# Performance work log

Measured on AMD Instinct MI355X. Metric: run time of the kernel, lower is better.

## Reference

```python
import jax, jax.numpy as jnp
import numpy as np

HEADS = 8
DIM_HEAD = 64


def setup_inputs() -> dict:
    key = jax.random.key(0)
    ks = jax.random.split(key, 6)
    B, Nq, Nk, Dq = 4, 2048, 2048, 1024
    inner = HEADS * DIM_HEAD  # 512
    return {
        "x": jax.random.normal(ks[0], (B, Nq, Dq), jnp.float32),
        "context": jax.random.normal(ks[1], (B, Nk, Dq), jnp.float32),
        "Wq": jax.random.normal(ks[2], (Dq, inner), jnp.float32) * 0.02,
        "Wkv": jax.random.normal(ks[3], (Dq, 2 * inner), jnp.float32) * 0.02,
        "Wout": jax.random.normal(ks[4], (inner, Dq), jnp.float32) * 0.02,
        "bout": jax.random.normal(ks[5], (Dq,), jnp.float32) * 0.02,
        "topk": 64,
    }


def reference(x, context, Wq, Wkv, Wout, bout, topk):
    B, Nq, _ = x.shape
    Nk = context.shape[1]
    H, D = HEADS, DIM_HEAD
    scale = D ** -0.5

    # projections: b n (h d) -> b h n d
    q = (x @ Wq).reshape(B, Nq, H, D).transpose(0, 2, 1, 3)
    kv = context @ Wkv
    k, v = jnp.split(kv, 2, axis=-1)
    k = k.reshape(B, Nk, H, D).transpose(0, 2, 1, 3)
    v = v.reshape(B, Nk, H, D).transpose(0, 2, 1, 3)

    sim = jnp.einsum('bhid,bhjd->bhij', q, k) * scale  # [B,H,Nq,Nk]

    # top-k sparsification: keep only topk keys per query, mask rest to -max
    k_eff = min(int(topk), Nk)
    _, idx = jax.lax.top_k(sim, k_eff)  # [B,H,Nq,k_eff]
    keep = jnp.zeros(sim.shape, dtype=bool)
    bi = jnp.arange(B)[:, None, None, None]
    hi = jnp.arange(H)[None, :, None, None]
    qi = jnp.arange(Nq)[None, None, :, None]
    keep = keep.at[bi, hi, qi, idx].set(True)
    max_neg = -jnp.finfo(sim.dtype).max
    sim = jnp.where(keep, sim, max_neg)

    attn = jax.nn.softmax(sim, axis=-1)
    out = jnp.einsum('bhij,bhjd->bhid', attn, v)
    out = out.transpose(0, 2, 1, 3).reshape(B, Nq, H * D)
    return out @ Wout + bout
```

## Files before the change

### kernel.cpp

```cpp
#include <hip/hip_runtime.h>
#include <math.h>

#define BATCH 4
#define NQ 2048
#define NK 2048
#define DQ 1024
#define NHEADS 8
#define DHEAD 64
#define INNER (NHEADS*DHEAD)
#define NROWS (BATCH*NHEADS*NQ)
#define CAND_MAX 128

using frag_ab = __attribute__((ext_vector_type(8))) short;
using frag_cd = __attribute__((ext_vector_type(4))) float;
using u16x8   = __attribute__((ext_vector_type(8))) unsigned short;

static __device__ __forceinline__ unsigned short f32_to_bf16_rne(float f) {
  unsigned u = __float_as_uint(f);
  u += 0x7FFFu + ((u >> 16) & 1u);
  return (unsigned short)(u >> 16);
}

static __device__ __forceinline__ void split_trunc(float f, unsigned short& h, unsigned short& l) {
  unsigned u = __float_as_uint(f);
  h = (unsigned short)(u >> 16);
  float hf = __uint_as_float(u & 0xFFFF0000u);
  unsigned r = __float_as_uint(f - hf);
  l = (unsigned short)(r >> 16);
}

static __device__ __forceinline__ void split3(float f, unsigned short& h,
                                              unsigned short& m, unsigned short& l) {
  unsigned u = __float_as_uint(f);
  h = (unsigned short)(u >> 16);
  float hf = __uint_as_float(u & 0xFFFF0000u);
  float r1 = f - hf;
  unsigned u1 = __float_as_uint(r1);
  m = (unsigned short)(u1 >> 16);
  float mf = __uint_as_float(u1 & 0xFFFF0000u);
  float r2 = r1 - mf;
  l = (unsigned short)(__float_as_uint(r2) >> 16);
}

__global__ __launch_bounds__(256) void split_wT3(
    const float* __restrict__ W, int ldw, int coloff, int K, int N,
    unsigned short* __restrict__ TH, unsigned short* __restrict__ TM,
    unsigned short* __restrict__ TL)
{
  __shared__ float tile[32*33];
  const int k0 = blockIdx.x * 32, n0 = blockIdx.y * 32;
  const int t = threadIdx.x;
  {
    int lk = t >> 3, ln4 = (t & 7) * 4;
    const float4 v = *(const float4*)(W + (size_t)(k0 + lk)*ldw + coloff + n0 + ln4);
    tile[lk*33 + ln4+0] = v.x;
    tile[lk*33 + ln4+1] = v.y;
    tile[lk*33 + ln4+2] = v.z;
    tile[lk*33 + ln4+3] = v.w;
  }
  __syncthreads();
  int n = t >> 3, k4 = (t & 7) * 4;
  #pragma unroll
  for (int j = 0; j < 4; ++j) {
    unsigned short h, m, l;
    split3(tile[(k4+j)*33 + n], h, m, l);
    size_t o = (size_t)(n0 + n)*K + k0 + k4 + j;
    TH[o] = h; TM[o] = m; TL[o] = l;
  }
}

__global__ __launch_bounds__(256) void split_wT(
    const float* __restrict__ W, int ldw, int coloff, int K, int N,
    unsigned short* __restrict__ TH, unsigned short* __restrict__ TL)
{
  __shared__ float tile[32*33];
  const int k0 = blockIdx.x * 32, n0 = blockIdx.y * 32;
  const int t = threadIdx.x;
  {
    int lk = t >> 3, ln4 = (t & 7) * 4;
    const float4 v = *(const float4*)(W + (size_t)(k0 + lk)*ldw + coloff + n0 + ln4);
    tile[lk*33 + ln4+0] = v.x;
    tile[lk*33 + ln4+1] = v.y;
    tile[lk*33 + ln4+2] = v.z;
    tile[lk*33 + ln4+3] = v.w;
  }
  __syncthreads();
  int n = t >> 3, k4 = (t & 7) * 4;
  #pragma unroll
  for (int j = 0; j < 4; ++j) {
    unsigned short h, l;
    split_trunc(tile[(k4+j)*33 + n], h, l);
    TH[(size_t)(n0 + n)*K + k0 + k4 + j] = h;
    TL[(size_t)(n0 + n)*K + k0 + k4 + j] = l;
  }
}

__global__ __launch_bounds__(512) void gemm_mfma6_proj(
    const float* __restrict__ A0,
    const unsigned short* __restrict__ BtH0, const unsigned short* __restrict__ BtM0,
    const unsigned short* __restrict__ BtL0,
    float* __restrict__ C0_, unsigned short* __restrict__ Hi0, unsigned short* __restrict__ Lo0,
    const float* __restrict__ A1,
    const unsigned short* __restrict__ BtH1, const unsigned short* __restrict__ BtM1,
    const unsigned short* __restrict__ BtL1,
    float* __restrict__ C1_, unsigned short* __restrict__ Hi1, unsigned short* __restrict__ Lo1)
{
  extern __shared__ unsigned short smp[];
  unsigned short* ah = smp;
  unsigned short* am = ah + 128*40;
  unsigned short* al = am + 128*40;
  unsigned short* bh = al + 128*40;
  unsigned short* bm = bh + 128*40;
  unsigned short* bl = bm + 128*40;

  const int t = threadIdx.x;
  const int w = t >> 6, l = t & 63;
  const int lr = l & 15, quad = l >> 4;
  const int bid = (int)blockIdx.x;
  const int half = bid >> 8;
  const int b2 = bid & 255;
  const int lid = (b2 & 7) * 32 + (b2 >> 3);
  const int n0 = (lid & 3) * 128, m0 = (lid >> 2) * 128;

  const float* A = half ? A1 : A0;
  const unsigned short* BtH = half ? BtH1 : BtH0;
  const unsigned short* BtM = half ? BtM1 : BtM0;
  const unsigned short* BtL = half ? BtL1 : BtL0;
  float* C32 = half ? C1_ : C0_;
  unsigned short* Hi = half ? Hi1 : Hi0;
  unsigned short* Lo = half ? Lo1 : Lo0;

  frag_cd acc[8];
  #pragma unroll
  for (int nt = 0; nt < 8; ++nt)
    acc[nt] = (frag_cd){0.f, 0.f, 0.f, 0.f};

  for (int kt = 0; kt < DQ; kt += 32) {
    {
      int row = t >> 2, k8 = (t & 3) * 8;
      const float* src = A + (size_t)(m0 + row) * DQ + kt + k8;
      float4 v0 = *(const float4*)(src);
      float4 v1 = *(const float4*)(src + 4);
      float vv[8] = {v0.x, v0.y, v0.z, v0.w, v1.x, v1.y, v1.z, v1.w};
      unsigned short h8[8], m8[8], l8[8];
      #pragma unroll
      for (int j = 0; j < 8; ++j) split3(vv[j], h8[j], m8[j], l8[j]);
      *(u16x8*)(ah + row*40 + k8) = *(u16x8*)h8;
      *(u16x8*)(am + row*40 + k8) = *(u16x8*)m8;
      *(u16x8*)(al + row*40 + k8) = *(u16x8*)l8;
    }
    {
      int n = t >> 2, k8 = (t & 3) * 8;
      size_t o = (size_t)(n0 + n)*DQ + kt + k8;
      *(u16x8*)(bh + n*40 + k8) = *(const u16x8*)(BtH + o);
      *(u16x8*)(bm + n*40 + k8) = *(const u16x8*)(BtM + o);
      *(u16x8*)(bl + n*40 + k8) = *(const u16x8*)(BtL + o);
    }
    __syncthreads();
    {
      int row = w*16 + lr;
      frag_ab aH = *(const frag_ab*)(ah + row*40 + quad*8);
      frag_ab aM = *(const frag_ab*)(am + row*40 + quad*8);
      frag_ab aL = *(const frag_ab*)(al + row*40 + quad*8);
      #pragma unroll
      for (int nt = 0; nt < 8; ++nt) {
        int bn = nt*16 + lr;
        frag_ab bH_ = *(const frag_ab*)(bh + bn*40 + quad*8);
        frag_ab bM_ = *(const frag_ab*)(bm + bn*40 + quad*8);
        frag_ab bL_ = *(const frag_ab*)(bl + bn*40 + quad*8);
        frag_cd c = acc[nt];
        c = __builtin_amdgcn_mfma_f32_16x16x32_bf16(aL, bH_, c, 0, 0, 0);
        c = __builtin_amdgcn_mfma_f32_16x16x32_bf16(aH, bL_, c, 0, 0, 0);
        c = __builtin_amdgcn_mfma_f32_16x16x32_bf16(aM, bM_, c, 0, 0, 0);
        c = __builtin_amdgcn_mfma_f32_16x16x32_bf16(aM, bH_, c, 0, 0, 0);
        c = __builtin_amdgcn_mfma_f32_16x16x32_bf16(aH, bM_, c, 0, 0, 0);
        c = __builtin_amdgcn_mfma_f32_16x16x32_bf16(aH, bH_, c, 0, 0, 0);
        acc[nt] = c;
      }
    }
    __syncthreads();
  }

  #pragma unroll
  for (int nt = 0; nt < 8; ++nt) {
    int cc = n0 + nt*16 + lr;
    int h = cc >> 6, d = cc & 63;
    #pragma unroll
    for (int i = 0; i < 4; ++i) {
      int r = m0 + w*16 + quad*4 + i;
      int b = r >> 11, n = r & (NQ - 1);
      size_t idx = (((size_t)(b*NHEADS + h))*NQ + n)*64 + d;
      float vf = acc[nt][i];
      C32[idx] = vf;
      unsigned short hb = f32_to_bf16_rne(vf);
      float hf = __uint_as_float((unsigned)hb << 16);
      unsigned short lb = f32_to_bf16_rne(vf - hf);
      Hi[idx] = hb;
      Lo[idx] = lb;
    }
  }
}

template<int MODE>
__global__ __launch_bounds__(512) void gemm_mfma3(
    const float* __restrict__ A, int lda,
    const unsigned short* __restrict__ BtH, const unsigned short* __restrict__ BtL,
    int K, int N, const float* __restrict__ bias, float* __restrict__ C0)
{
  __shared__ unsigned short ah[128*40];
  __shared__ unsigned short al[128*40];
  __shared__ unsigned short bh2[128*40];
  __shared__ unsigned short bl2[128*40];
  const int t = threadIdx.x;
  const int w = t >> 6, l = t & 63;
  const int lr = l & 15, quad = l >> 4;
  const int nx = N >> 7;
  const int bid = (int)blockIdx.x;
  const int nwg = (int)gridDim.x;
  const int lid = (bid & 7) * (nwg >> 3) + (bid >> 3);
  const int n0 = (lid % nx) * 128, m0 = (lid / nx) * 128;

  frag_cd acc[8];
  #pragma unroll
  for (int nt = 0; nt < 8; ++nt)
    acc[nt] = (frag_cd){0.f, 0.f, 0.f, 0.f};

  for (int kt = 0; kt < K; kt += 32) {
    {
      int row = t >> 2, k8 = (t & 3) * 8;
      const float* src = A + (size_t)(m0 + row) * lda + kt + k8;
      float4 v0 = *(const float4*)(src);
      float4 v1 = *(const float4*)(src + 4);
      float vv[8] = {v0.x, v0.y, v0.z, v0.w, v1.x, v1.y, v1.z, v1.w};
      unsigned short h8[8], l8[8];
      #pragma unroll
      for (int j = 0; j < 8; ++j) split_trunc(vv[j], h8[j], l8[j]);
      *(u16x8*)(ah + row*40 + k8) = *(u16x8*)h8;
      *(u16x8*)(al + row*40 + k8) = *(u16x8*)l8;
    }
    {
      int n = t >> 2, k8 = (t & 3) * 8;
      size_t o = (size_t)(n0 + n)*K + kt + k8;
      *(u16x8*)(bh2 + n*40 + k8) = *(const u16x8*)(BtH + o);
      *(u16x8*)(bl2 + n*40 + k8) = *(const u16x8*)(BtL + o);
    }
    __syncthreads();
    {
      int row = w*16 + lr;
      frag_ab aH = *(const frag_ab*)(ah + row*40 + quad*8);
      frag_ab aL = *(const frag_ab*)(al + row*40 + quad*8);
      #pragma unroll
      for (int nt = 0; nt < 8; ++nt) {
        int bn = nt*16 + lr;
        frag_ab bH_ = *(const frag_ab*)(bh2 + bn*40 + quad*8);
        frag_ab bL_ = *(const frag_ab*)(bl2 + bn*40 + quad*8);
        acc[nt] = __builtin_amdgcn_mfma_f32_16x16x32_bf16(aH, bH_, acc[nt], 0, 0, 0);
        acc[nt] = __builtin_amdgcn_mfma_f32_16x16x32_bf16(aH, bL_, acc[nt], 0, 0, 0);
        acc[nt] = __builtin_amdgcn_mfma_f32_16x16x32_bf16(aL, bH_, acc[nt], 0, 0, 0);
      }
    }
    __syncthreads();
  }

  #pragma unroll
  for (int nt = 0; nt < 8; ++nt) {
    int cc = n0 + nt*16 + lr;
    #pragma unroll
    for (int i = 0; i < 4; ++i) {
      int r = m0 + w*16 + quad*4 + i;
      float v = acc[nt][i];
      if (MODE == 0) {
        C0[(size_t)r * N + cc] = v + bias[cc];
      } else {
        int b = r >> 11, n = r & (NQ - 1);
        int h = cc >> 6, d = cc & 63;
        C0[(((size_t)(b*NHEADS + h))*NK + n)*64 + d] = v;
      }
    }
  }
}

__global__ __launch_bounds__(512) void score_mfma(
    const unsigned short* __restrict__ Qhi, const unsigned short* __restrict__ Qlo,
    const unsigned short* __restrict__ Khi, const unsigned short* __restrict__ Klo,
    unsigned short* __restrict__ S16, int bh0)
{
  extern __shared__ unsigned short sm[];
  unsigned short* qh = sm;
  unsigned short* ql = qh + 128*72;
  unsigned short* kh = ql + 128*72;
  unsigned short* kl = kh + 128*72;

  const int t  = threadIdx.x;
  const int qt = blockIdx.x, kt = blockIdx.y;
  const int bh = bh0 + blockIdx.z;
  const size_t qbase = ((size_t)bh*NQ + qt*128) * 64;
  const size_t kbase = ((size_t)bh*NK + kt*128) * 64;

  #pragma unroll
  for (int i = 0; i < 2; ++i) {
    int c   = t + i*512;
    int row = c >> 3, off = (c & 7) * 8;
    *(u16x8*)(qh + row*72 + off) = *(const u16x8*)(Qhi + qbase + row*64 + off);
    *(u16x8*)(ql + row*72 + off) = *(const u16x8*)(Qlo + qbase + row*64 + off);
    *(u16x8*)(kh + row*72 + off) = *(const u16x8*)(Khi + kbase + row*64 + off);
    *(u16x8*)(kl + row*72 + off) = *(const u16x8*)(Klo + kbase + row*64 + off);
  }
  __syncthreads();

  const int w = t >> 6, l = t & 63;
  const int quad = l >> 4, lr = l & 15;

  frag_ab aH[2], aL[2];
  {
    int row = w*16 + lr;
    #pragma unroll
    for (int s = 0; s < 2; ++s) {
      aH[s] = *(const frag_ab*)(qh + row*72 + s*32 + quad*8);
      aL[s] = *(const frag_ab*)(ql + row*72 + s*32 + quad*8);
    }
  }

  for (int ks = 0; ks < 8; ++ks) {
    frag_ab bH[2], bL[2];
    int krow = ks*16 + lr;
    #pragma unroll
    for (int s = 0; s < 2; ++s) {
      bH[s] = *(const frag_ab*)(kh + krow*72 + s*32 + quad*8);
      bL[s] = *(const frag_ab*)(kl + krow*72 + s*32 + quad*8);
    }
    frag_cd c = {0.f, 0.f, 0.f, 0.f};
    #pragma unroll
    for (int s = 0; s < 2; ++s) {
      c = __builtin_amdgcn_mfma_f32_16x16x32_bf16(aH[s], bH[s], c, 0, 0, 0);
      c = __builtin_amdgcn_mfma_f32_16x16x32_bf16(aH[s], bL[s], c, 0, 0, 0);
      c = __builtin_amdgcn_mfma_f32_16x16x32_bf16(aL[s], bH[s], c, 0, 0, 0);
    }
    int qrow = qt*128 + w*16 + quad*4;
    int kcol = kt*128 + ks*16 + lr;
    size_t base = ((size_t)blockIdx.z * NQ + qrow) * NK + kcol;
    #pragma unroll
    for (int i = 0; i < 4; ++i) {
      _Float16 h = (_Float16)(c[i] * 0.125f);
      S16[base + (size_t)i*NK] = __builtin_bit_cast(unsigned short, h);
    }
  }
}

__global__ __launch_bounds__(256) void select_rows(
    const unsigned short* __restrict__ S16, unsigned short* __restrict__ cand,
    int* __restrict__ cnt, const int* __restrict__ topkp, int row0)
{
  const int t = threadIdx.x;
  const int w = t >> 6, l = t & 63;
  const int rl = blockIdx.x * 4 + w;
  const size_t row = (size_t)row0 + rl;
  const unsigned short* Sr = S16 + (size_t)rl * NK;
  const unsigned long long lmask = (1ull << l) - 1ull;

  int kEff = *topkp;
  if (kEff > CAND_MAX) kEff = CAND_MAX;
  if (kEff < 1) kEff = 1;

  unsigned uv[32];
  #pragma unroll
  for (int c = 0; c < 32; ++c) {
    unsigned bb = Sr[c*64 + l];
    uv[c] = (bb & 0x8000u) ? (~bb & 0xFFFFu) : (bb | 0x8000u);
  }
  unsigned lo_ = 0u, hi_ = 0xFFFFu;
  while (lo_ < hi_) {
    unsigned mid = (lo_ + hi_ + 1u) >> 1;
    int c_ = 0;
    #pragma unroll
    for (int c = 0; c < 32; ++c) c_ += (uv[c] >= mid) ? 1 : 0;
    #pragma unroll
    for (int off = 32; off > 0; off >>= 1) c_ += __shfl_xor(c_, off);
    if (c_ >= kEff) lo_ = mid; else hi_ = mid - 1;
  }
  unsigned short sb = (lo_ & 0x8000u) ? (unsigned short)(lo_ & 0x7FFFu)
                                      : (unsigned short)(~lo_ & 0xFFFFu);
  float skth = (float)__builtin_bit_cast(_Float16, sb);
  float smarg = skth - 3e-3f;
  _Float16 hm = (_Float16)smarg;
  unsigned short mb = __builtin_bit_cast(unsigned short, hm);
  unsigned um = (mb & 0x8000u) ? (~(unsigned)mb & 0xFFFFu) : ((unsigned)mb | 0x8000u);

  int base = 0;
  for (int c = 0; c < 32; ++c) {
    bool pred = (uv[c] >= um);
    unsigned long long msk = __ballot(pred);
    if (pred) {
      int pos = base + __popcll(msk & lmask);
      if (pos < CAND_MAX) cand[row*CAND_MAX + pos] = (unsigned short)(c*64 + l);
    }
    base += __popcll(msk);
  }
  if (l == 0) cnt[row] = (base < CAND_MAX) ? base : CAND_MAX;
}

__global__ __launch_bounds__(256) void attn_phase_b(
    const float* __restrict__ Q32, const float* __restrict__ K32,
    const float* __restrict__ V32, const unsigned short* __restrict__ cand,
    const int* __restrict__ cnt, float* __restrict__ inner,
    const int* __restrict__ topkp)
{
  __shared__ uint2 pvbuf[4][128];

  const int t = threadIdx.x;
  const int w = t >> 6, l = t & 63;
  const int nwg = (int)gridDim.x;
  const int bid = (int)blockIdx.x;
  const int swz = (bid & 7) * (nwg >> 3) + (bid >> 3);
  const size_t row = (size_t)swz * 4 + w;
  const int bh = (int)(row >> 11);
  const int q  = (int)(row & (NQ - 1));
  const unsigned long long lmask = (1ull << l) - 1ull;

  int kEff = *topkp;
  if (kEff > CAND_MAX) kEff = CAND_MAX;
  if (kEff < 1) kEff = 1;
  int m = cnt[row];
  if (kEff > m) kEff = m;

  const float* Kb = K32 + (size_t)bh * NK * 64;
  const float* Vb = V32 + (size_t)bh * NK * 64;

  const int g = l >> 3, r = l & 7;
  double2 q2[4];
  #pragma unroll
  for (int i = 0; i < 4; ++i) {
    float2 qf = *(const float2*)(Q32 + row*64 + i*16 + r*2);
    q2[i].x = (double)qf.x;
    q2[i].y = (double)qf.y;
  }

  int ck[2];
  ck[0] = cand[row*CAND_MAX + l];
  ck[1] = cand[row*CAND_MAX + 64 + l];
  double cs[2] = {-INFINITY, -INFINITY};
  unsigned long long cu[2] = {0ull, 0ull};

  #define RESCORE_PASS(P, C)                                                  \
  {                                                                           \
    const int j = (P)*8 + g;                                                  \
    const bool valid = (j < m);                                               \
    int key = __shfl(ck[C], j & 63);                                          \
    const float* kp = Kb + (size_t)(valid ? key : 0) * 64;                    \
    double s0 = 0.0, s1 = 0.0;                                                \
    _Pragma("unroll")                                                         \
    for (int i = 0; i < 4; ++i) {                                             \
      float2 kv = *(const float2*)(kp + i*16 + r*2);                          \
      s0 = fma((double)kv.x, q2[i].x, s0);                                    \
      s1 = fma((double)kv.y, q2[i].y, s1);                                    \
    }                                                                         \
    double s = s0 + s1;                                                       \
    s += __shfl_xor(s, 1);                                                    \
    s += __shfl_xor(s, 2);                                                    \
    s += __shfl_xor(s, 4);                                                    \
    s *= 0.125;                                                               \
    double sc = __shfl(s, (l & 7) * 8);                                       \
    const int pp = (P) & 7;                                                   \
    if ((l >> 3) == pp && ((C)*64 + pp*8 + (l & 7)) < m) {                    \
      unsigned long long b = (unsigned long long)__double_as_longlong(sc);    \
      cs[C] = sc;                                                             \
      cu[C] = (b >> 63) ? ~b : (b | 0x8000000000000000ull);                   \
    }                                                                         \
  }

  if (m <= 64) {
    #pragma unroll
    for (int p = 0; p < 8; ++p) RESCORE_PASS(p, 0)
  } else {
    #pragma unroll
    for (int p = 0; p < 8; ++p) RESCORE_PASS(p, 0)
    const int np2 = 8 + ((m - 64 + 7) >> 3);
    for (int p = 8; p < np2; ++p) RESCORE_PASS(p, 1)
  }
  #undef RESCORE_PASS

  const unsigned hu0 = (unsigned)(cu[0] >> 32), lu0 = (unsigned)cu[0];
  const unsigned hu1 = (unsigned)(cu[1] >> 32), lu1 = (unsigned)cu[1];

  unsigned T32 = 0u;
  for (int bit = 31; bit >= 0; --bit) {
    unsigned cT = T32 | (1u << bit);
    int tot = __popcll(__ballot(hu0 >= cT)) + __popcll(__ballot(hu1 >= cT));
    if (tot >= kEff) T32 = cT;
  }
  unsigned Tlo;
  {
    int cgt32 = __popcll(__ballot(hu0 > T32)) + __popcll(__ballot(hu1 > T32));
    bool e0 = (hu0 == T32), e1 = (hu1 == T32);
    unsigned long long bm0 = __ballot(e0), bm1 = __ballot(e1);
    int ceq = __popcll(bm0) + __popcll(bm1);
    int nEq32 = kEff - cgt32;
    if (ceq == 1) {
      Tlo = bm0 ? __shfl(lu0, (int)__builtin_ctzll(bm0))
                : __shfl(lu1, (int)__builtin_ctzll(bm1));
    } else {
      unsigned TL = 0u;
      for (int bit = 31; bit >= 0; --bit) {
        unsigned cT = TL | (1u << bit);
        int tot = __popcll(__ballot(e0 && lu0 >= cT))
                + __popcll(__ballot(e1 && lu1 >= cT));
        if (tot >= nEq32) TL = cT;
      }
      Tlo = TL;
    }
  }
  const unsigned long long T = ((unsigned long long)T32 << 32) | Tlo;

  double s_kth;
  { unsigned long long bb = (T >> 63) ? (T & 0x7FFFFFFFFFFFFFFFull) : ~T;
    s_kth = __longlong_as_double((long long)bb); }

  double nx = -INFINITY;
  #pragma unroll
  for (int c = 0; c < 2; ++c) { double v = (cu[c] < T) ? cs[c] : -INFINITY; nx = fmax(nx, v); }
  #pragma unroll
  for (int off = 32; off > 0; off >>= 1) nx = fmax(nx, __shfl_xor(nx, off));

  double smax = fmax(cs[0], cs[1]);
  #pragma unroll
  for (int off = 32; off > 0; off >>= 1) smax = fmax(smax, __shfl_xor(smax, off));

  const double DELTA = 5e-6;
  float wgt[2];
  if (!(s_kth - nx < 2.0*DELTA)) {
    int cgt = __popcll(__ballot(cu[0] > T)) + __popcll(__ballot(cu[1] > T));
    int nEq = kEff - cgt;
    int eqBase = 0;
    #pragma unroll
    for (int c = 0; c < 2; ++c) {
      bool eq = (cu[c] == T);
      unsigned long long eqm = __ballot(eq);
      int er = __popcll(eqm & lmask);
      bool sel = (cu[c] > T) || (eq && (eqBase + er) < nEq);
      eqBase += __popcll(eqm);
      wgt[c] = sel ? expf((float)(cs[c] - smax)) : 0.f;
    }
  } else {
    double cmid = 0.5 * (s_kth + nx);
    #pragma unroll
    for (int c = 0; c < 2; ++c) {
      double mu = 0.5 + (cs[c] - cmid) / (2.0*DELTA);
      mu = fmin(1.0, fmax(0.0, mu));
      wgt[c] = (float)mu * expf((float)(cs[c] - smax));
    }
  }

  pvbuf[w][l]      = make_uint2((unsigned)ck[0] & (NK - 1), __float_as_uint(wgt[0]));
  pvbuf[w][64 + l] = make_uint2((unsigned)ck[1] & (NK - 1), __float_as_uint(wgt[1]));
  float wsum = wgt[0] + wgt[1];
  #pragma unroll
  for (int off = 32; off > 0; off >>= 1) wsum += __shfl_xor(wsum, off);
  asm volatile("s_waitcnt lgkmcnt(0)" ::: "memory");

  const int sub = l >> 4;
  const int dl  = l & 15;
  const float* Vb4 = Vb + dl * 4;
  float ax = 0.f, ay = 0.f, az = 0.f, aw = 0.f;
  const int mm4 = (m + 3) & ~3;
  #pragma unroll 4
  for (int j0 = 0; j0 < mm4; j0 += 4) {
    uint2 p = pvbuf[w][j0 + sub];
    float wj = __uint_as_float(p.y);
    const float4 v = *(const float4*)(Vb4 + ((size_t)p.x << 6));
    ax = fmaf(wj, v.x, ax);
    ay = fmaf(wj, v.y, ay);
    az = fmaf(wj, v.z, az);
    aw = fmaf(wj, v.w, aw);
  }
  #pragma unroll
  for (int off = 32; off >= 16; off >>= 1) {
    ax += __shfl_xor(ax, off);
    ay += __shfl_xor(ay, off);
    az += __shfl_xor(az, off);
    aw += __shfl_xor(aw, off);
  }
  if (sub == 0) {
    int b = bh >> 3, h = bh & 7;
    float inv = 1.0f / wsum;
    float4 o;
    o.x = ax * inv; o.y = ay * inv; o.z = az * inv; o.w = aw * inv;
    *(float4*)(inner + ((size_t)b*NQ + q)*INNER + h*DHEAD + dl*4) = o;
  }
}

extern "C" void kernel_launch(void* const* d_in, const int* in_sizes, int n_in,
                              void* d_out, int out_size, void* d_ws, size_t ws_size,
                              hipStream_t stream)
{
  const float* x    = (const float*)d_in[0];
  const float* ctx  = (const float*)d_in[1];
  const float* Wq   = (const float*)d_in[2];
  const float* Wkv  = (const float*)d_in[3];
  const float* Wout = (const float*)d_in[4];
  const float* bout = (const float*)d_in[5];
  const int*   topk = (const int*)d_in[6];
  float* out = (float*)d_out;

  const size_t SZ = (size_t)BATCH * NHEADS * NQ * DHEAD;

  size_t off = 0;
  char* base = (char*)d_ws;
  auto take = [&](size_t bytes) { char* r = base + off; off += (bytes + 255) & ~(size_t)255; return r; };
  float* Q32 = (float*)take(SZ * sizeof(float));
  float* K32 = (float*)take(SZ * sizeof(float));
  unsigned short* cand = (unsigned short*)take((size_t)NROWS * CAND_MAX * 2);
  int* cnt = (int*)take((size_t)NROWS * sizeof(int));
  unsigned short* Qhi = (unsigned short*)take(SZ * 2);
  unsigned short* Qlo = (unsigned short*)take(SZ * 2);
  unsigned short* Khi = (unsigned short*)take(SZ * 2);
  unsigned short* Klo = (unsigned short*)take(SZ * 2);
  char* slab = base + off;

  const size_t WSZ = (size_t)INNER * DQ * 2;
  unsigned short* WqTH = (unsigned short*)(slab + 0*WSZ);
  unsigned short* WqTM = (unsigned short*)(slab + 1*WSZ);
  unsigned short* WqTL = (unsigned short*)(slab + 2*WSZ);
  unsigned short* WkTH = (unsigned short*)(slab + 3*WSZ);
  unsigned short* WkTM = (unsigned short*)(slab + 4*WSZ);
  unsigned short* WkTL = (unsigned short*)(slab + 5*WSZ);
  unsigned short* S16 = (unsigned short*)slab;
  unsigned short* WvTH = (unsigned short*)(slab + 0*WSZ);
  unsigned short* WvTL = (unsigned short*)(slab + 1*WSZ);
  unsigned short* WoTH = (unsigned short*)(slab + 2*WSZ);
  unsigned short* WoTL = (unsigned short*)(slab + 3*WSZ);
  float* V32   = (float*)Qhi;
  float* inner = (float*)Khi;

  const size_t per_bh = (size_t)NQ * NK * sizeof(unsigned short);
  size_t avail = (ws_size > off) ? (ws_size - off) : 0;
  int bhchunk = (int)(avail / per_bh);
  if (bhchunk < 1)  bhchunk = 1;
  if (bhchunk > 32) bhchunk = 32;

  const int M = BATCH * NQ;
  const int SCORE_LDS = 4 * 128 * 72 * (int)sizeof(unsigned short);
  const int PROJ_LDS  = 6 * 128 * 40 * (int)sizeof(unsigned short);
  hipFuncSetAttribute(reinterpret_cast<const void*>(score_mfma),
                      hipFuncAttributeMaxDynamicSharedMemorySize, SCORE_LDS);
  hipFuncSetAttribute(reinterpret_cast<const void*>(gemm_mfma6_proj),
                      hipFuncAttributeMaxDynamicSharedMemorySize, PROJ_LDS);

  split_wT3<<<dim3(DQ/32, INNER/32), 256, 0, stream>>>(Wq,  INNER,   0, DQ, INNER, WqTH, WqTM, WqTL);
  split_wT3<<<dim3(DQ/32, INNER/32), 256, 0, stream>>>(Wkv, 2*INNER, 0, DQ, INNER, WkTH, WkTM, WkTL);

  gemm_mfma6_proj<<<dim3(512), 512, PROJ_LDS, stream>>>(
      x,   WqTH, WqTM, WqTL, Q32, Qhi, Qlo,
      ctx, WkTH, WkTM, WkTL, K32, Khi, Klo);

  for (int c0 = 0; c0 < BATCH*NHEADS; c0 += bhchunk) {
    int cc = BATCH*NHEADS - c0; if (cc > bhchunk) cc = bhchunk;
    score_mfma<<<dim3(NQ/128, NK/128, cc), 512, SCORE_LDS, stream>>>(
        Qhi, Qlo, Khi, Klo, S16, c0);
    select_rows<<<dim3(cc*NQ/4), 256, 0, stream>>>(S16, cand, cnt, topk, c0*NQ);
  }

  split_wT<<<dim3(DQ/32, INNER/32), 256, 0, stream>>>(Wkv, 2*INNER, INNER, DQ, INNER, WvTH, WvTL);
  split_wT<<<dim3(INNER/32, DQ/32), 256, 0, stream>>>(Wout, DQ, 0, INNER, DQ, WoTH, WoTL);

  gemm_mfma3<2><<<dim3((INNER/128)*(M/128)), 512, 0, stream>>>(ctx, DQ, WvTH, WvTL, DQ, INNER, nullptr, V32);
  attn_phase_b<<<dim3(NROWS/4), 256, 0, stream>>>(Q32, K32, V32, cand, cnt, inner, topk);
  gemm_mfma3<0><<<dim3((DQ/128)*(M/128)), 512, 0, stream>>>(inner, INNER, WoTH, WoTL, INNER, DQ, bout, out);
}
```

Measured before the change: 708.8 us.

## Fuse score computation with top-k selection, keeping score rows in LDS

Merges the score GEMM and row-wise threshold selection into one kernel. Each block computes a 16-query by 2048-key score strip and holds it in shared memory, then runs the binary-search selection directly from LDS. This removes the large fp16 score matrix round trip through global memory and the chunked launch loop. In exchange, K fragments are read straight from global memory with no LDS reuse across query tiles, and each block uses about 70 KB of LDS, which limits occupancy.

```diff
diff --git a/kernel.cpp b/kernel.cpp
--- a/kernel.cpp
+++ b/kernel.cpp
@@ -280,54 +280,56 @@
   }
 }
 
-__global__ __launch_bounds__(512) void score_mfma(
+#define SC_STRIDE 2056
+__global__ __launch_bounds__(512) void score_select_fused(
     const unsigned short* __restrict__ Qhi, const unsigned short* __restrict__ Qlo,
     const unsigned short* __restrict__ Khi, const unsigned short* __restrict__ Klo,
-    unsigned short* __restrict__ S16, int bh0)
+    unsigned short* __restrict__ cand, int* __restrict__ cnt,
+    const int* __restrict__ topkp)
 {
-  extern __shared__ unsigned short sm[];
-  unsigned short* qh = sm;
-  unsigned short* ql = qh + 128*72;
-  unsigned short* kh = ql + 128*72;
-  unsigned short* kl = kh + 128*72;
-
-  const int t  = threadIdx.x;
-  const int qt = blockIdx.x, kt = blockIdx.y;
-  const int bh = bh0 + blockIdx.z;
-  const size_t qbase = ((size_t)bh*NQ + qt*128) * 64;
-  const size_t kbase = ((size_t)bh*NK + kt*128) * 64;
-
-  #pragma unroll
-  for (int i = 0; i < 2; ++i) {
-    int c   = t + i*512;
-    int row = c >> 3, off = (c & 7) * 8;
-    *(u16x8*)(qh + row*72 + off) = *(const u16x8*)(Qhi + qbase + row*64 + off);
-    *(u16x8*)(ql + row*72 + off) = *(const u16x8*)(Qlo + qbase + row*64 + off);
-    *(u16x8*)(kh + row*72 + off) = *(const u16x8*)(Khi + kbase + row*64 + off);
-    *(u16x8*)(kl + row*72 + off) = *(const u16x8*)(Klo + kbase + row*64 + off);
-  }
-  __syncthreads();
-
+  extern __shared__ unsigned short smf[];
+  unsigned short* qh = smf;
+  unsigned short* ql = qh + 16*72;
+  unsigned short* sc = ql + 16*72;
+
+  const int t = threadIdx.x;
   const int w = t >> 6, l = t & 63;
   const int quad = l >> 4, lr = l & 15;
+  const unsigned long long lmask = (1ull << l) - 1ull;
+
+  const int bid = (int)blockIdx.x;
+  const int lid = (bid & 7) * 512 + (bid >> 3);
+  const int bh  = lid >> 7;
+  const int grp = lid & 127;
+
+  const size_t qbase = ((size_t)bh*NQ + grp*16) * 64;
+  const size_t kbase = (size_t)bh * NK * 64;
+
+  if (t < 256) {
+    int arr = t >> 7;
+    int c = t & 127;
+    int row = c >> 3, off = (c & 7) * 8;
+    const unsigned short* srcp = (arr ? Qlo : Qhi) + qbase + row*64 + off;
+    unsigned short* dstp = (arr ? ql : qh) + row*72 + off;
+    *(u16x8*)dstp = *(const u16x8*)srcp;
+  }
+  __syncthreads();
 
   frag_ab aH[2], aL[2];
-  {
-    int row = w*16 + lr;
+  #pragma unroll
+  for (int s = 0; s < 2; ++s) {
+    aH[s] = *(const frag_ab*)(qh + lr*72 + s*32 + quad*8);
+    aL[s] = *(const frag_ab*)(ql + lr*72 + s*32 + quad*8);
+  }
+
+  for (int kt8 = 0; kt8 < 16; ++kt8) {
+    const int ktile = kt8*8 + w;
+    const int krow  = ktile*16 + lr;
+    frag_ab bH[2], bL[2];
     #pragma unroll
     for (int s = 0; s < 2; ++s) {
-      aH[s] = *(const frag_ab*)(qh + row*72 + s*32 + quad*8);
-      aL[s] = *(const frag_ab*)(ql + row*72 + s*32 + quad*8);
-    }
-  }
-
-  for (int ks = 0; ks < 8; ++ks) {
-    frag_ab bH[2], bL[2];
-    int krow = ks*16 + lr;
-    #pragma unroll
-    for (int s = 0; s < 2; ++s) {
-      bH[s] = *(const frag_ab*)(kh + krow*72 + s*32 + quad*8);
-      bL[s] = *(const frag_ab*)(kl + krow*72 + s*32 + quad*8);
+      bH[s] = *(const frag_ab*)(Khi + kbase + (size_t)krow*64 + s*32 + quad*8);
+      bL[s] = *(const frag_ab*)(Klo + kbase + (size_t)krow*64 + s*32 + quad*8);
     }
     frag_cd c = {0.f, 0.f, 0.f, 0.f};
     #pragma unroll
@@ -336,67 +338,60 @@
       c = __builtin_amdgcn_mfma_f32_16x16x32_bf16(aH[s], bL[s], c, 0, 0, 0);
       c = __builtin_amdgcn_mfma_f32_16x16x32_bf16(aL[s], bH[s], c, 0, 0, 0);
     }
-    int qrow = qt*128 + w*16 + quad*4;
-    int kcol = kt*128 + ks*16 + lr;
-    size_t base = ((size_t)blockIdx.z * NQ + qrow) * NK + kcol;
+    const int kcol = ktile*16 + lr;
     #pragma unroll
     for (int i = 0; i < 4; ++i) {
       _Float16 h = (_Float16)(c[i] * 0.125f);
-      S16[base + (size_t)i*NK] = __builtin_bit_cast(unsigned short, h);
-    }
-  }
-}
-
-__global__ __launch_bounds__(256) void select_rows(
-    const unsigned short* __restrict__ S16, unsigned short* __restrict__ cand,
-    int* __restrict__ cnt, const int* __restrict__ topkp, int row0)
-{
-  const int t = threadIdx.x;
-  const int w = t >> 6, l = t & 63;
-  const int rl = blockIdx.x * 4 + w;
-  const size_t row = (size_t)row0 + rl;
-  const unsigned short* Sr = S16 + (size_t)rl * NK;
-  const unsigned long long lmask = (1ull << l) - 1ull;
+      sc[(quad*4 + i)*SC_STRIDE + kcol] = __builtin_bit_cast(unsigned short, h);
+    }
+  }
+  __syncthreads();
 
   int kEff = *topkp;
   if (kEff > CAND_MAX) kEff = CAND_MAX;
   if (kEff < 1) kEff = 1;
 
-  unsigned uv[32];
-  #pragma unroll
-  for (int c = 0; c < 32; ++c) {
-    unsigned bb = Sr[c*64 + l];
-    uv[c] = (bb & 0x8000u) ? (~bb & 0xFFFFu) : (bb | 0x8000u);
-  }
-  unsigned lo_ = 0u, hi_ = 0xFFFFu;
-  while (lo_ < hi_) {
-    unsigned mid = (lo_ + hi_ + 1u) >> 1;
-    int c_ = 0;
-    #pragma unroll
-    for (int c = 0; c < 32; ++c) c_ += (uv[c] >= mid) ? 1 : 0;
-    #pragma unroll
-    for (int off = 32; off > 0; off >>= 1) c_ += __shfl_xor(c_, off);
-    if (c_ >= kEff) lo_ = mid; else hi_ = mid - 1;
-  }
-  unsigned short sb = (lo_ & 0x8000u) ? (unsigned short)(lo_ & 0x7FFFu)
-                                      : (unsigned short)(~lo_ & 0xFFFFu);
-  float skth = (float)__builtin_bit_cast(_Float16, sb);
-  float smarg = skth - 3e-3f;
-  _Float16 hm = (_Float16)smarg;
-  unsigned short mb = __builtin_bit_cast(unsigned short, hm);
-  unsigned um = (mb & 0x8000u) ? (~(unsigned)mb & 0xFFFFu) : ((unsigned)mb | 0x8000u);
-
-  int base = 0;
-  for (int c = 0; c < 32; ++c) {
-    bool pred = (uv[c] >= um);
-    unsigned long long msk = __ballot(pred);
-    if (pred) {
-      int pos = base + __popcll(msk & lmask);
-      if (pos < CAND_MAX) cand[row*CAND_MAX + pos] = (unsigned short)(c*64 + l);
-    }
-    base += __popcll(msk);
-  }
-  if (l == 0) cnt[row] = (base < CAND_MAX) ? base : CAND_MAX;
+  for (int rr = 0; rr < 2; ++rr) {
+    const int r = w*2 + rr;
+    const unsigned short* Sr = sc + r*SC_STRIDE;
+    const size_t row = (size_t)bh*NQ + grp*16 + r;
+
+    unsigned uv[32];
+    #pragma unroll
+    for (int c = 0; c < 32; ++c) {
+      unsigned bb = Sr[c*64 + l];
+      uv[c] = (bb & 0x8000u) ? (~bb & 0xFFFFu) : (bb | 0x8000u);
+    }
+    unsigned lo_ = 0u, hi_ = 0xFFFFu;
+    while (lo_ < hi_) {
+      unsigned mid = (lo_ + hi_ + 1u) >> 1;
+      int c_ = 0;
+      #pragma unroll
+      for (int c = 0; c < 32; ++c) c_ += (uv[c] >= mid) ? 1 : 0;
+      #pragma unroll
+      for (int off = 32; off > 0; off >>= 1) c_ += __shfl_xor(c_, off);
+      if (c_ >= kEff) lo_ = mid; else hi_ = mid - 1;
+    }
+    unsigned short sb = (lo_ & 0x8000u) ? (unsigned short)(lo_ & 0x7FFFu)
+                                        : (unsigned short)(~lo_ & 0xFFFFu);
+    float skth = (float)__builtin_bit_cast(_Float16, sb);
+    float smarg = skth - 3e-3f;
+    _Float16 hm = (_Float16)smarg;
+    unsigned short mb = __builtin_bit_cast(unsigned short, hm);
+    unsigned um = (mb & 0x8000u) ? (~(unsigned)mb & 0xFFFFu) : ((unsigned)mb | 0x8000u);
+
+    int base = 0;
+    for (int c = 0; c < 32; ++c) {
+      bool pred = (uv[c] >= um);
+      unsigned long long msk = __ballot(pred);
+      if (pred) {
+        int pos = base + __popcll(msk & lmask);
+        if (pos < CAND_MAX) cand[row*CAND_MAX + pos] = (unsigned short)(c*64 + l);
+      }
+      base += __popcll(msk);
+    }
+    if (l == 0) cnt[row] = (base < CAND_MAX) ? base : CAND_MAX;
+  }
 }
 
 __global__ __launch_bounds__(256) void attn_phase_b(
@@ -623,7 +618,6 @@
   unsigned short* WkTH = (unsigned short*)(slab + 3*WSZ);
   unsigned short* WkTM = (unsigned short*)(slab + 4*WSZ);
   unsigned short* WkTL = (unsigned short*)(slab + 5*WSZ);
-  unsigned short* S16 = (unsigned short*)slab;
   unsigned short* WvTH = (unsigned short*)(slab + 0*WSZ);
   unsigned short* WvTL = (unsigned short*)(slab + 1*WSZ);
   unsigned short* WoTH = (unsigned short*)(slab + 2*WSZ);
@@ -631,19 +625,13 @@
   float* V32   = (float*)Qhi;
   float* inner = (float*)Khi;
 
-  const size_t per_bh = (size_t)NQ * NK * sizeof(unsigned short);
-  size_t avail = (ws_size > off) ? (ws_size - off) : 0;
-  int bhchunk = (int)(avail / per_bh);
-  if (bhchunk < 1)  bhchunk = 1;
-  if (bhchunk > 32) bhchunk = 32;
-
   const int M = BATCH * NQ;
-  const int SCORE_LDS = 4 * 128 * 72 * (int)sizeof(unsigned short);
   const int PROJ_LDS  = 6 * 128 * 40 * (int)sizeof(unsigned short);
-  hipFuncSetAttribute(reinterpret_cast<const void*>(score_mfma),
-                      hipFuncAttributeMaxDynamicSharedMemorySize, SCORE_LDS);
+  const int FUSE_LDS  = (2*16*72 + 16*SC_STRIDE) * (int)sizeof(unsigned short);
   hipFuncSetAttribute(reinterpret_cast<const void*>(gemm_mfma6_proj),
                       hipFuncAttributeMaxDynamicSharedMemorySize, PROJ_LDS);
+  hipFuncSetAttribute(reinterpret_cast<const void*>(score_select_fused),
+                      hipFuncAttributeMaxDynamicSharedMemorySize, FUSE_LDS);
 
   split_wT3<<<dim3(DQ/32, INNER/32), 256, 0, stream>>>(Wq,  INNER,   0, DQ, INNER, WqTH, WqTM, WqTL);
   split_wT3<<<dim3(DQ/32, INNER/32), 256, 0, stream>>>(Wkv, 2*INNER, 0, DQ, INNER, WkTH, WkTM, WkTL);
@@ -652,12 +640,8 @@
       x,   WqTH, WqTM, WqTL, Q32, Qhi, Qlo,
       ctx, WkTH, WkTM, WkTL, K32, Khi, Klo);
 
-  for (int c0 = 0; c0 < BATCH*NHEADS; c0 += bhchunk) {
-    int cc = BATCH*NHEADS - c0; if (cc > bhchunk) cc = bhchunk;
-    score_mfma<<<dim3(NQ/128, NK/128, cc), 512, SCORE_LDS, stream>>>(
-        Qhi, Qlo, Khi, Klo, S16, c0);
-    select_rows<<<dim3(cc*NQ/4), 256, 0, stream>>>(S16, cand, cnt, topk, c0*NQ);
-  }
+  score_select_fused<<<dim3(4096), 512, FUSE_LDS, stream>>>(
+      Qhi, Qlo, Khi, Klo, cand, cnt, topk);
 
   split_wT<<<dim3(DQ/32, INNER/32), 256, 0, stream>>>(Wkv, 2*INNER, INNER, DQ, INNER, WvTH, WvTL);
   split_wT<<<dim3(INNER/32, DQ/32), 256, 0, stream>>>(Wout, DQ, 0, INNER, DQ, WoTH, WoTL);
```

Measured after the change: 754.4 us. 1.06x slower.
